# Kernel tuning notes

Hardware: AMD Instinct MI355X
Metric: run time of the kernel (lower is better)

## Reference

```python
import jax, jax.numpy as jnp
import numpy as np

# module config (init_kwargs)
AH, AW = 14, 14            # aligned_height, aligned_width
SCALE = 0.25               # spatial_scale
RATIO = 2                  # sampling_ratio
SHIFT = 0.0                # spatial_shift (added in feature-map coords)
HALF_PART = 0              # 0 = full box
ROI_SCALE = 1.0            # box rescale about its center


def setup_inputs() -> dict:
    key = jax.random.key(0)
    kf, kb, kx, ky, kw, kh = jax.random.split(key, 6)
    B, C, H, W = 2, 256, 200, 272
    N = 256
    features = jax.random.normal(kf, (B, C, H, W), dtype=jnp.float32)
    img_h, img_w = H / SCALE, W / SCALE
    bidx = jax.random.randint(kb, (N,), 0, B).astype(jnp.float32)
    x1 = jax.random.uniform(kx, (N,)) * (img_w * 0.6)
    y1 = jax.random.uniform(ky, (N,)) * (img_h * 0.6)
    bw = 32.0 + jax.random.uniform(kw, (N,)) * (img_w * 0.35)
    bh = 32.0 + jax.random.uniform(kh, (N,)) * (img_h * 0.35)
    rois = jnp.stack([bidx, x1, y1, x1 + bw, y1 + bh], axis=1).astype(jnp.float32)
    return {"features": features, "rois": rois}


def _lin_idx(coord, size):
    # bilinear index/weight prep with RoIAlign boundary rules
    valid = (coord > -1.0) & (coord < float(size))
    c = jnp.clip(coord, 0.0, float(size - 1))
    lo = jnp.floor(c)
    hi = jnp.minimum(lo + 1.0, float(size - 1))
    frac = c - lo
    return lo.astype(jnp.int32), hi.astype(jnp.int32), frac, valid.astype(coord.dtype)


def _roi_mask_align(features, rois):
    B, C, H, W = features.shape
    N = rois.shape[0]
    PH, PW, r = AH + 1, AW + 1, RATIO
    b = rois[:, 0].astype(jnp.int32)
    # to feature-map coords, with roi_scale about the box center and spatial_shift
    x1, y1, x2, y2 = (rois[:, 1] * SCALE, rois[:, 2] * SCALE,
                      rois[:, 3] * SCALE, rois[:, 4] * SCALE)
    cx, cy = 0.5 * (x1 + x2), 0.5 * (y1 + y2)
    hw, hh = 0.5 * (x2 - x1) * ROI_SCALE, 0.5 * (y2 - y1) * ROI_SCALE
    x1, x2 = cx - hw + SHIFT, cx + hw + SHIFT
    y1, y2 = cy - hh + SHIFT, cy + hh + SHIFT
    roi_w = jnp.maximum(x2 - x1, 1.0)
    roi_h = jnp.maximum(y2 - y1, 1.0)
    bin_w = roi_w / PW
    bin_h = roi_h / PH
    # sample coords, separable: sx [N, PW*r], sy [N, PH*r]
    ix = jnp.arange(PW * r, dtype=jnp.float32)
    iy = jnp.arange(PH * r, dtype=jnp.float32)
    sx = x1[:, None] + (ix[None, :] + 0.5) * (bin_w[:, None] / r)
    sy = y1[:, None] + (iy[None, :] + 0.5) * (bin_h[:, None] / r)
    y_lo, y_hi, fy, vy = _lin_idx(sy, H)
    x_lo, x_hi, fx, vx = _lin_idx(sx, W)
    featsT = jnp.transpose(features, (0, 2, 3, 1))  # [B,H,W,C]
    bb = b[:, None, None]
    gather = lambda yi, xi: featsT[bb, yi[:, :, None], xi[:, None, :]]  # [N,Sy,Sx,C]
    wy0, wy1 = 1.0 - fy, fy
    wx0, wx1 = 1.0 - fx, fx
    val = (gather(y_lo, x_lo) * (wy0[:, :, None] * wx0[:, None, :])[..., None]
           + gather(y_lo, x_hi) * (wy0[:, :, None] * wx1[:, None, :])[..., None]
           + gather(y_hi, x_lo) * (wy1[:, :, None] * wx0[:, None, :])[..., None]
           + gather(y_hi, x_hi) * (wy1[:, :, None] * wx1[:, None, :])[..., None])
    val = val * (vy[:, :, None] * vx[:, None, :])[..., None]
    # average the r*r samples per bin -> [N, PH, PW, C]
    val = val.reshape(N, PH, r, PW, r, C).mean(axis=(2, 4))
    return jnp.transpose(val, (0, 3, 1, 2))  # [N, C, PH, PW]


def reference(features, rois):
    x = _roi_mask_align(features, rois)  # [N, C, AH+1, AW+1]
    # avg_pool2d(kernel=2, stride=1)
    out = 0.25 * (x[..., :-1, :-1] + x[..., 1:, :-1]
                  + x[..., :-1, 1:] + x[..., 1:, 1:])
    return out  # [N, C, AH, AW]
```

## Files before the change

### kernel.cpp

```cpp
#include <hip/hip_runtime.h>


#define AH_  14
#define AW_  14
#define C_   256
#define H_   200
#define W_   272
#define HW_  (H_ * W_)
#define CPB  4

#define GLOAD_LDS16(g, l)                                                     \
  __builtin_amdgcn_global_load_lds(                                           \
      (const __attribute__((address_space(1))) void*)(g),                     \
      (__attribute__((address_space(3))) void*)(l), 16, 0, 0)

__global__ __launch_bounds__(128, 8)
void roi_mask_align_avg_kernel(const float* __restrict__ feat,
                               const float* __restrict__ rois,
                               float* __restrict__ out) {
    __shared__ float Ls[2][1024];

    const int p   = blockIdx.x;
    const int xcd = p & 7;
    const int q   = p >> 3;
    const int n   = q & 255;
    const int cgi = q >> 8;
    const int cg  = cgi * 8 + xcd;
    const int c0  = cg * CPB;

    const int tid  = threadIdx.x;
    const int wave = tid >> 6;
    const int lane = tid & 63;
    const int half = lane >> 5;
    const int ix   = lane & 31;

    float* __restrict__ LsW = Ls[wave];

    const float r0f = rois[n * 5 + 0];
    const float x1s = rois[n * 5 + 1] * 0.25f;
    const float y1s = rois[n * 5 + 2] * 0.25f;
    const float x2s = rois[n * 5 + 3] * 0.25f;
    const float y2s = rois[n * 5 + 4] * 0.25f;
    const int   b   = (int)r0f;

    const float cx = 0.5f * (x1s + x2s), cy = 0.5f * (y1s + y2s);
    const float hw = 0.5f * (x2s - x1s), hh = 0.5f * (y2s - y1s);
    const float x1 = cx - hw, x2 = cx + hw;
    const float y1 = cy - hh, y2 = cy + hh;
    const float roi_w = fmaxf(x2 - x1, 1.0f);
    const float roi_h = fmaxf(y2 - y1, 1.0f);
    const float sub_w = roi_w * (1.0f / 15.0f) * 0.5f;
    const float sub_h = roi_h * (1.0f / 15.0f) * 0.5f;

    const float sx  = x1 + ((float)ix + 0.5f) * sub_w;
    const bool  vx_ = (sx > -1.0f) && (sx < (float)W_) && (ix < 30);
    const float ccx = fminf(fmaxf(sx, 0.0f), (float)(W_ - 1));
    const float lox = floorf(ccx);
    const int   xl  = (int)lox;
    const int   xh  = min(xl + 1, W_ - 1);
    const float fx  = ccx - lox;
    const float vmx = vx_ ? 1.0f : 0.0f;
    const float wx0 = (1.0f - fx) * vmx;
    const float wx1 = fx * vmx;

    const int s0    = __builtin_amdgcn_readfirstlane(xl);
    const int s0c   = min(s0, W_ - 128);
    const int xh29  = __builtin_amdgcn_readlane(xh, 29);
    const int spanh = xh29 - s0c;
    const bool ldact = (ix * 4) <= spanh;
    const int iA    = half * 128 + (vx_ ? (xl - s0c) : 0);

    const float* __restrict__ bpA = feat + ((size_t)b * C_ + c0) * (size_t)HW_;
    const float* __restrict__ gAl = bpA + (size_t)half * HW_ + s0c + 4 * ix;
    const float* __restrict__ gBl = gAl + 2 * HW_;

    const int  aw   = ix >> 1;
    const bool emit = ((lane & 1) == 0) && (aw < AW_);
    const int  iy0  = wave * 14;

    const int   l    = lane & 15;
    const float syl  = y1 + ((float)(iy0 + l) + 0.5f) * sub_h;
    const bool  vyl  = (syl > -1.0f) && (syl < (float)H_);
    const float ccyl = fminf(fmaxf(syl, 0.0f), (float)(H_ - 1));
    const float loyl = floorf(ccyl);
    const float fyl  = ccyl - loyl;
    const float vmyl = vyl ? 1.0f : 0.0f;
    const int   yll  = (int)loyl;
    const int   yhl  = min(yll + 1, H_ - 1);
    const int   wy0b = __float_as_int((1.0f - fyl) * vmyl);
    const int   wy1b = __float_as_int(fyl * vmyl);
    const int   olol = yll * W_;
    const int   ohil = yhl * W_;
    const int   pyll = __shfl_up(yll, 1, 64);
    const int   pyhl = __shfl_up(yhl, 1, 64);
    const int   casel = (l == 0) ? 2
                       : (yll == pyll) ? 0
                       : (yll == pyhl) ? 1 : 2;

    float alo0 = 0.f, alo1 = 0.f, ahi0 = 0.f, ahi1 = 0.f;
    float blo0 = 0.f, blo1 = 0.f, bhi0 = 0.f, bhi1 = 0.f;
    float outA[7], outB[7];
    float prevSA = 0.f, prevSB = 0.f, PA = 0.f, PB = 0.f;

    #pragma unroll
    for (int i = 0; i < 16; ++i) {
        const int   sc  = __builtin_amdgcn_readlane(casel, i);
        const float wy0 = __int_as_float(__builtin_amdgcn_readlane(wy0b, i));
        const float wy1 = __int_as_float(__builtin_amdgcn_readlane(wy1b, i));

        if (sc == 1) {
            alo0 = ahi0; alo1 = ahi1; blo0 = bhi0; blo1 = bhi1;
            const int ohi = __builtin_amdgcn_readlane(ohil, i);
            asm volatile("s_waitcnt lgkmcnt(0)" ::: "memory");
            if (ldact) {
                GLOAD_LDS16(gAl + ohi, LsW + 512);
                GLOAD_LDS16(gBl + ohi, LsW + 768);
            }
            asm volatile("s_waitcnt vmcnt(0)" ::: "memory");
            ahi0 = LsW[512 + iA]; ahi1 = LsW[512 + iA + 1];
            bhi0 = LsW[768 + iA]; bhi1 = LsW[768 + iA + 1];
        } else if (sc == 2) {
            const int olo = __builtin_amdgcn_readlane(olol, i);
            const int ohi = __builtin_amdgcn_readlane(ohil, i);
            asm volatile("s_waitcnt lgkmcnt(0)" ::: "memory");
            if (ldact) {
                GLOAD_LDS16(gAl + olo, LsW);
                GLOAD_LDS16(gBl + olo, LsW + 256);
                GLOAD_LDS16(gAl + ohi, LsW + 512);
                GLOAD_LDS16(gBl + ohi, LsW + 768);
            }
            asm volatile("s_waitcnt vmcnt(0)" ::: "memory");
            alo0 = LsW[iA];       alo1 = LsW[iA + 1];
            blo0 = LsW[256 + iA]; blo1 = LsW[256 + iA + 1];
            ahi0 = LsW[512 + iA]; ahi1 = LsW[512 + iA + 1];
            bhi0 = LsW[768 + iA]; bhi1 = LsW[768 + iA + 1];
        }

        const float w00 = wy0 * wx0, w01 = wy0 * wx1;
        const float w10 = wy1 * wx0, w11 = wy1 * wx1;
        PA += alo0 * w00 + alo1 * w01 + ahi0 * w10 + ahi1 * w11;
        PB += blo0 * w00 + blo1 * w01 + bhi0 * w10 + bhi1 * w11;

        if (i & 1) {
            const float tA = PA + __shfl_xor(PA, 1, 64);
            const float uA = tA + __shfl_down(tA, 2, 64);
            const float tB = PB + __shfl_xor(PB, 1, 64);
            const float uB = tB + __shfl_down(tB, 2, 64);
            const int kk = i >> 1;
            if (kk > 0) {
                outA[kk - 1] = (prevSA + uA) * 0.0625f;
                outB[kk - 1] = (prevSB + uB) * 0.0625f;
            }
            prevSA = uA; prevSB = uB;
            PA = 0.f; PB = 0.f;
        }
    }

    if (emit) {
        #pragma unroll
        for (int k = 0; k < 7; ++k) {
            LsW[half * 98 + k * AW_ + aw]       = outA[k];
            LsW[(2 + half) * 98 + k * AW_ + aw] = outB[k];
        }
    }
    float* __restrict__ op = out + ((size_t)n * C_ + c0) * (AH_ * AW_);
    for (int o = lane; o < CPB * 7 * AW_; o += 64) {
        const int ch  = o / 98;
        const int rem = o - ch * 98;
        op[ch * (AH_ * AW_) + wave * 98 + rem] = LsW[o];
    }
}

extern "C" void kernel_launch(void* const* d_in, const int* in_sizes, int n_in,
                              void* d_out, int out_size, void* d_ws, size_t ws_size,
                              hipStream_t stream) {
    const float* feat = (const float*)d_in[0];
    const float* rois = (const float*)d_in[1];
    float* out = (float*)d_out;
    const int grid = 256 * (C_ / CPB);
    roi_mask_align_avg_kernel<<<grid, 128, 0, stream>>>(feat, rois, out);
}
```

Baseline: 245.2 us.

## Double-buffer LDS row loads to prefetch next sample row during compute

Each wave now has two LDS buffers. The loads for sample row i+1 are issued before row i is consumed, with partial vmcnt waits, so global-to-LDS latency overlaps the bilinear accumulation instead of stalling every iteration. The first row is prefetched before the loop. LDS use per block doubles, and the explicit min-blocks occupancy hint is dropped, which may change register allocation and occupancy.

Result: faster. 227.8 us (-7.1%).

```diff
diff --git a/kernel.cpp b/kernel.cpp
--- a/kernel.cpp
+++ b/kernel.cpp
@@ -14,11 +14,11 @@
       (const __attribute__((address_space(1))) void*)(g),                     \
       (__attribute__((address_space(3))) void*)(l), 16, 0, 0)
 
-__global__ __launch_bounds__(128, 8)
+__global__ __launch_bounds__(128)
 void roi_mask_align_avg_kernel(const float* __restrict__ feat,
                                const float* __restrict__ rois,
                                float* __restrict__ out) {
-    __shared__ float Ls[2][1024];
+    __shared__ float Ls[2][2048];
 
     const int p   = blockIdx.x;
     const int xcd = p & 7;
@@ -97,6 +97,17 @@
                        : (yll == pyll) ? 0
                        : (yll == pyhl) ? 1 : 2;
 
+    {
+        const int olo = __builtin_amdgcn_readlane(olol, 0);
+        const int ohi = __builtin_amdgcn_readlane(ohil, 0);
+        if (ldact) {
+            GLOAD_LDS16(gAl + olo, LsW);
+            GLOAD_LDS16(gBl + olo, LsW + 256);
+            GLOAD_LDS16(gAl + ohi, LsW + 512);
+            GLOAD_LDS16(gBl + ohi, LsW + 768);
+        }
+    }
+
     float alo0 = 0.f, alo1 = 0.f, ahi0 = 0.f, ahi1 = 0.f;
     float blo0 = 0.f, blo1 = 0.f, bhi0 = 0.f, bhi1 = 0.f;
     float outA[7], outB[7];
@@ -104,36 +115,49 @@
 
     #pragma unroll
     for (int i = 0; i < 16; ++i) {
-        const int   sc  = __builtin_amdgcn_readlane(casel, i);
+        if (i < 15) {
+            const int scn = __builtin_amdgcn_readlane(casel, i + 1);
+            float* bn = LsW + ((i + 1) & 1) * 1024;
+            if (scn == 2) {
+                const int olo_n = __builtin_amdgcn_readlane(olol, i + 1);
+                const int ohi_n = __builtin_amdgcn_readlane(ohil, i + 1);
+                asm volatile("s_waitcnt lgkmcnt(0)" ::: "memory");
+                if (ldact) {
+                    GLOAD_LDS16(gAl + olo_n, bn);
+                    GLOAD_LDS16(gBl + olo_n, bn + 256);
+                    GLOAD_LDS16(gAl + ohi_n, bn + 512);
+                    GLOAD_LDS16(gBl + ohi_n, bn + 768);
+                }
+                asm volatile("s_waitcnt vmcnt(4)" ::: "memory");
+            } else if (scn == 1) {
+                const int ohi_n = __builtin_amdgcn_readlane(ohil, i + 1);
+                asm volatile("s_waitcnt lgkmcnt(0)" ::: "memory");
+                if (ldact) {
+                    GLOAD_LDS16(gAl + ohi_n, bn + 512);
+                    GLOAD_LDS16(gBl + ohi_n, bn + 768);
+                }
+                asm volatile("s_waitcnt vmcnt(2)" ::: "memory");
+            } else {
+                asm volatile("s_waitcnt vmcnt(0)" ::: "memory");
+            }
+        } else {
+            asm volatile("s_waitcnt vmcnt(0)" ::: "memory");
+        }
+
+        const int   sci = __builtin_amdgcn_readlane(casel, i);
         const float wy0 = __int_as_float(__builtin_amdgcn_readlane(wy0b, i));
         const float wy1 = __int_as_float(__builtin_amdgcn_readlane(wy1b, i));
-
-        if (sc == 1) {
+        const float* d  = LsW + (i & 1) * 1024;
+
+        if (sci == 1) {
             alo0 = ahi0; alo1 = ahi1; blo0 = bhi0; blo1 = bhi1;
-            const int ohi = __builtin_amdgcn_readlane(ohil, i);
-            asm volatile("s_waitcnt lgkmcnt(0)" ::: "memory");
-            if (ldact) {
-                GLOAD_LDS16(gAl + ohi, LsW + 512);
-                GLOAD_LDS16(gBl + ohi, LsW + 768);
-            }
-            asm volatile("s_waitcnt vmcnt(0)" ::: "memory");
-            ahi0 = LsW[512 + iA]; ahi1 = LsW[512 + iA + 1];
-            bhi0 = LsW[768 + iA]; bhi1 = LsW[768 + iA + 1];
-        } else if (sc == 2) {
-            const int olo = __builtin_amdgcn_readlane(olol, i);
-            const int ohi = __builtin_amdgcn_readlane(ohil, i);
-            asm volatile("s_waitcnt lgkmcnt(0)" ::: "memory");
-            if (ldact) {
-                GLOAD_LDS16(gAl + olo, LsW);
-                GLOAD_LDS16(gBl + olo, LsW + 256);
-                GLOAD_LDS16(gAl + ohi, LsW + 512);
-                GLOAD_LDS16(gBl + ohi, LsW + 768);
-            }
-            asm volatile("s_waitcnt vmcnt(0)" ::: "memory");
-            alo0 = LsW[iA];       alo1 = LsW[iA + 1];
-            blo0 = LsW[256 + iA]; blo1 = LsW[256 + iA + 1];
-            ahi0 = LsW[512 + iA]; ahi1 = LsW[512 + iA + 1];
-            bhi0 = LsW[768 + iA]; bhi1 = LsW[768 + iA + 1];
+            ahi0 = d[512 + iA]; ahi1 = d[512 + iA + 1];
+            bhi0 = d[768 + iA]; bhi1 = d[768 + iA + 1];
+        } else if (sci == 2) {
+            alo0 = d[iA];       alo1 = d[iA + 1];
+            blo0 = d[256 + iA]; blo1 = d[256 + iA + 1];
+            ahi0 = d[512 + iA]; ahi1 = d[512 + iA + 1];
+            bhi0 = d[768 + iA]; bhi1 = d[768 + iA + 1];
         }
 
         const float w00 = wy0 * wx0, w01 = wy0 * wx1;
```
